# Kernel tuning notes

Measured on AMD Instinct MI355X. Metric: run time of the kernel, lower is better.

Reference implementation:

```python
import jax, jax.numpy as jnp
import numpy as np

H = 15  # hidden_dim


def _lstm_layer(x_seq, w_ih, w_hh, b_ih, b_hh):
    """One LSTM layer, PyTorch gate order (i, f, g, o).
    x_seq: (T, B, D_in) -> returns output sequence (T, B, H)."""
    T, B, _ = x_seq.shape
    # Precompute input contribution for all timesteps at once: (T, B, 4H)
    xw = jnp.einsum('tbd,gd->tbg', x_seq, w_ih) + b_ih + b_hh

    def step(carry, xw_t):
        h, c = carry
        gates = xw_t + h @ w_hh.T  # (B, 4H)
        i, f, g, o = jnp.split(gates, 4, axis=-1)
        i = jax.nn.sigmoid(i)
        f = jax.nn.sigmoid(f)
        g = jnp.tanh(g)
        o = jax.nn.sigmoid(o)
        c = f * c + i * g
        h = o * jnp.tanh(c)
        return (h, c), h

    h0 = jnp.zeros((B, H), dtype=x_seq.dtype)
    c0 = jnp.zeros((B, H), dtype=x_seq.dtype)
    _, out = jax.lax.scan(step, (h0, c0), xw)
    return out  # (T, B, H)


def setup_inputs() -> dict:
    key = jax.random.key(0)
    ks = jax.random.split(key, 11)
    D, OUT = 5, 25
    s = 0.1
    return {
        'x':     jax.random.normal(ks[0], (512, 4096, D), dtype=jnp.float32),
        'w_ih0': jax.random.normal(ks[1], (4 * H, D), dtype=jnp.float32) * s,
        'w_hh0': jax.random.normal(ks[2], (4 * H, H), dtype=jnp.float32) * s,
        'b_ih0': jax.random.normal(ks[3], (4 * H,), dtype=jnp.float32) * s,
        'b_hh0': jax.random.normal(ks[4], (4 * H,), dtype=jnp.float32) * s,
        'w_ih1': jax.random.normal(ks[5], (4 * H, H), dtype=jnp.float32) * s,
        'w_hh1': jax.random.normal(ks[6], (4 * H, H), dtype=jnp.float32) * s,
        'b_ih1': jax.random.normal(ks[7], (4 * H,), dtype=jnp.float32) * s,
        'b_hh1': jax.random.normal(ks[8], (4 * H,), dtype=jnp.float32) * s,
        'w_lin': jax.random.normal(ks[9], (OUT, H), dtype=jnp.float32) * s,
        'b_lin': jax.random.normal(ks[10], (OUT,), dtype=jnp.float32) * s,
    }


def reference(x, w_ih0, w_hh0, b_ih0, b_hh0, w_ih1, w_hh1, b_ih1, b_hh1, w_lin, b_lin):
    out0 = _lstm_layer(x, w_ih0, w_hh0, b_ih0, b_hh0)      # (T, B, H)
    out1 = _lstm_layer(out0, w_ih1, w_hh1, b_ih1, b_hh1)   # (T, B, H)
    # Faithful to the source: output[:, -1, :] with seq-first layout selects
    # the last BATCH element across all timesteps -> (T, H)
    last = out1[:, -1, :]
    return last @ w_lin.T + b_lin  # (T, OUT)
```

## Files before the change

kernel.cpp:

```cpp
#include <hip/hip_runtime.h>

#define T_SEQ 512
#define BATCH 4096
#define D_IN  5
#define H     15
#define G4    60
#define OUTN  25

__device__ __forceinline__ float fast_exp2(float x) {
#if __has_builtin(__builtin_amdgcn_exp2f)
  return __builtin_amdgcn_exp2f(x);
#else
  return exp2f(x);
#endif
}

__device__ __forceinline__ float fast_rcp(float x) {
#if __has_builtin(__builtin_amdgcn_rcpf)
  return __builtin_amdgcn_rcpf(x);
#else
  return 1.0f / x;
#endif
}

__device__ __forceinline__ float rl(float v, int lane) {
  return __int_as_float(__builtin_amdgcn_readlane(__float_as_int(v), lane));
}

template <int K>
__device__ __forceinline__ float qbcast(float v) {
  return __int_as_float(__builtin_amdgcn_update_dpp(
      0, __float_as_int(v), K * 0x55, 0xF, 0xF, true));
}

__global__ void precompute_xw0(const float* __restrict__ x,
                               const float* __restrict__ w_ih0,
                               const float* __restrict__ b_ih0,
                               const float* __restrict__ b_hh0,
                               float* __restrict__ xw0) {
  int idx = blockIdx.x * blockDim.x + threadIdx.x;
  if (idx >= T_SEQ * G4) return;
  int t = idx / G4;
  int g = idx - t * G4;
  const float* xp = x + ((size_t)t * BATCH + (BATCH - 1)) * D_IN;
  float a = b_ih0[g] + b_hh0[g];
#pragma unroll
  for (int d = 0; d < D_IN; ++d) a = fmaf(xp[d], w_ih0[g * D_IN + d], a);
  xw0[idx] = a;
}

__global__ void __launch_bounds__(64, 1)
lstm_serial(const float* __restrict__ xw0,
            const float* __restrict__ w_hh0,
            const float* __restrict__ w_ih1,
            const float* __restrict__ w_hh1,
            const float* __restrict__ b_ih1,
            const float* __restrict__ b_hh1,
            const float* __restrict__ w_lin,
            const float* __restrict__ b_lin,
            float* __restrict__ out) {
  const int lane = threadIdx.x;
  const int ty = lane & 3;
  const int j  = lane >> 2;
  const int g  = (j < H) ? (ty * H + j) : 0;

  float w0[H], wi1[H], wh1[H];
#pragma unroll
  for (int k = 0; k < H; ++k) {
    w0[k]  = w_hh0[g * H + k];
    wi1[k] = w_ih1[g * H + k];
    wh1[k] = w_hh1[g * H + k];
  }
  const float bias1 = b_ih1[g] + b_hh1[g];

  float wl[H];
  {
    int o = (lane < OUTN) ? lane : 0;
#pragma unroll
    for (int k = 0; k < H; ++k) wl[k] = w_lin[o * H + k];
  }
  const float bl = b_lin[(lane < OUTN) ? lane : 0];

  const bool  isT  = (ty == 2);
  const float expc = isT ? -2.8853900817779268f : -1.4426950408889634f;
  const float sc   = isT ? 2.0f : 1.0f;
  const float off  = isT ? -1.0f : 0.0f;
  const float TANH_C = -2.8853900817779268f;

  float c0 = 0.0f, c1 = 0.0f;
  float sh0[H], sh1[H];
#pragma unroll
  for (int k = 0; k < H; ++k) { sh0[k] = 0.0f; sh1[k] = 0.0f; }

  float xw_cur = xw0[g];
  float xw_n1  = xw0[1 * G4 + g];

  for (int t = 0; t < T_SEQ; ++t) {
    int tn = (t + 2 < T_SEQ) ? (t + 2) : 0;
    float xw_n2 = xw0[tn * G4 + g];

    float u3 = 0.0f, u4 = 0.0f, u5 = 0.0f;
#pragma unroll
    for (int k = 0; k < 5; ++k)   u3 = fmaf(wh1[k], sh1[k], u3);
#pragma unroll
    for (int k = 5; k < 10; ++k)  u4 = fmaf(wh1[k], sh1[k], u4);
#pragma unroll
    for (int k = 10; k < 15; ++k) u5 = fmaf(wh1[k], sh1[k], u5);

    float a0 = xw_cur, a1 = 0.0f, a2 = 0.0f;
#pragma unroll
    for (int k = 0; k < 5; ++k)   a0 = fmaf(w0[k], sh0[k], a0);
#pragma unroll
    for (int k = 5; k < 10; ++k)  a1 = fmaf(w0[k], sh0[k], a1);
#pragma unroll
    for (int k = 10; k < 15; ++k) a2 = fmaf(w0[k], sh0[k], a2);
    float a = a0 + (a1 + a2);

    float e = fast_exp2(a * expc);
    float s = fast_rcp(1.0f + e);
    float v = fmaf(s, sc, off);

    float vi = qbcast<0>(v), vf = qbcast<1>(v), vg = qbcast<2>(v), vo = qbcast<3>(v);
    c0 = fmaf(vf, c0, vi * vg);
    float ec = fast_exp2(c0 * TANH_C);
    float th = fmaf(fast_rcp(1.0f + ec), 2.0f, -1.0f);
    float h0v = vo * th;

#pragma unroll
    for (int k = 0; k < H; ++k) sh0[k] = rl(h0v, 4 * k);

    float u0 = bias1, u1 = 0.0f, u2 = 0.0f;
#pragma unroll
    for (int k = 0; k < 5; ++k)   u0 = fmaf(wi1[k], sh0[k], u0);
#pragma unroll
    for (int k = 5; k < 10; ++k)  u1 = fmaf(wi1[k], sh0[k], u1);
#pragma unroll
    for (int k = 10; k < 15; ++k) u2 = fmaf(wi1[k], sh0[k], u2);
    float b = ((u0 + u1) + (u2 + u3)) + (u4 + u5);

    float eb = fast_exp2(b * expc);
    float sb = fast_rcp(1.0f + eb);
    float vb = fmaf(sb, sc, off);

    float qi = qbcast<0>(vb), qf = qbcast<1>(vb), qg = qbcast<2>(vb), qo = qbcast<3>(vb);
    c1 = fmaf(qf, c1, qi * qg);
    float ec1 = fast_exp2(c1 * TANH_C);
    float th1 = fmaf(fast_rcp(1.0f + ec1), 2.0f, -1.0f);
    float h1v = qo * th1;

#pragma unroll
    for (int k = 0; k < H; ++k) sh1[k] = rl(h1v, 4 * k);

    float o0 = bl, o1 = 0.0f, o2 = 0.0f;
#pragma unroll
    for (int k = 0; k < 5; ++k)   o0 = fmaf(wl[k], sh1[k], o0);
#pragma unroll
    for (int k = 5; k < 10; ++k)  o1 = fmaf(wl[k], sh1[k], o1);
#pragma unroll
    for (int k = 10; k < 15; ++k) o2 = fmaf(wl[k], sh1[k], o2);
    if (lane < OUTN) out[t * OUTN + lane] = o0 + (o1 + o2);

    xw_cur = xw_n1;
    xw_n1  = xw_n2;
  }
}

extern "C" void kernel_launch(void* const* d_in, const int* in_sizes, int n_in,
                              void* d_out, int out_size, void* d_ws, size_t ws_size,
                              hipStream_t stream) {
  const float* x     = (const float*)d_in[0];
  const float* w_ih0 = (const float*)d_in[1];
  const float* w_hh0 = (const float*)d_in[2];
  const float* b_ih0 = (const float*)d_in[3];
  const float* b_hh0 = (const float*)d_in[4];
  const float* w_ih1 = (const float*)d_in[5];
  const float* w_hh1 = (const float*)d_in[6];
  const float* b_ih1 = (const float*)d_in[7];
  const float* b_hh1 = (const float*)d_in[8];
  const float* w_lin = (const float*)d_in[9];
  const float* b_lin = (const float*)d_in[10];
  float* out = (float*)d_out;
  float* xw0 = (float*)d_ws;

  precompute_xw0<<<dim3((T_SEQ * G4 + 255) / 256), dim3(256), 0, stream>>>(
      x, w_ih0, b_ih0, b_hh0, xw0);
  lstm_serial<<<dim3(1), dim3(64), 0, stream>>>(
      xw0, w_hh0, w_ih1, w_hh1, b_ih1, b_hh1, w_lin, b_lin, out);
}
```

Measured before the change: 291.2 us.

## Skew LSTM layers across timesteps and fold activation scales into weights

After: 236.9 us. 1.23x faster.

```diff
diff --git a/kernel.cpp b/kernel.cpp
--- a/kernel.cpp
+++ b/kernel.cpp
@@ -6,6 +6,10 @@
 #define H     15
 #define G4    60
 #define OUTN  25
+
+#define LOG2E   1.4426950408889634f
+#define M_SIG  (-1.4426950408889634f)
+#define M_TANH (-2.8853901f)
 
 __device__ __forceinline__ float fast_exp2(float x) {
 #if __has_builtin(__builtin_amdgcn_exp2f)
@@ -46,7 +50,8 @@
   float a = b_ih0[g] + b_hh0[g];
 #pragma unroll
   for (int d = 0; d < D_IN; ++d) a = fmaf(xp[d], w_ih0[g * D_IN + d], a);
-  xw0[idx] = a;
+  float m = (g / H == 2) ? M_TANH : M_SIG;
+  xw0[idx] = a * m;
 }
 
 __global__ void __launch_bounds__(64, 1)
@@ -64,14 +69,19 @@
   const int j  = lane >> 2;
   const int g  = (j < H) ? (ty * H + j) : 0;
 
+  const bool  isT = (ty == 2);
+  const float m   = isT ? M_TANH : M_SIG;
+  const float scv  = isT ? (2.0f * M_TANH) : 1.0f;
+  const float offv = isT ? (-M_TANH) : 0.0f;
+
   float w0[H], wi1[H], wh1[H];
 #pragma unroll
   for (int k = 0; k < H; ++k) {
-    w0[k]  = w_hh0[g * H + k];
-    wi1[k] = w_ih1[g * H + k];
-    wh1[k] = w_hh1[g * H + k];
+    w0[k]  = w_hh0[g * H + k] * m;
+    wi1[k] = w_ih1[g * H + k] * m;
+    wh1[k] = w_hh1[g * H + k] * m;
   }
-  const float bias1 = b_ih1[g] + b_hh1[g];
+  const float bias1 = (b_ih1[g] + b_hh1[g]) * m;
 
   float wl[H];
   {
@@ -81,88 +91,92 @@
   }
   const float bl = b_lin[(lane < OUTN) ? lane : 0];
 
-  const bool  isT  = (ty == 2);
-  const float expc = isT ? -2.8853900817779268f : -1.4426950408889634f;
-  const float sc   = isT ? 2.0f : 1.0f;
-  const float off  = isT ? -1.0f : 0.0f;
-  const float TANH_C = -2.8853900817779268f;
-
   float c0 = 0.0f, c1 = 0.0f;
   float sh0[H], sh1[H];
 #pragma unroll
   for (int k = 0; k < H; ++k) { sh0[k] = 0.0f; sh1[k] = 0.0f; }
 
+  float h0v = 0.0f, h1v = 0.0f;
+
+  auto L0 = [&](float xw) {
+    float a0 = xw, a1 = 0.0f, a2 = 0.0f;
+#pragma unroll
+    for (int k = 0; k < 5; ++k)   a0 = fmaf(w0[k], sh0[k], a0);
+#pragma unroll
+    for (int k = 5; k < 10; ++k)  a1 = fmaf(w0[k], sh0[k], a1);
+#pragma unroll
+    for (int k = 10; k < 15; ++k) a2 = fmaf(w0[k], sh0[k], a2);
+    float a = a0 + (a1 + a2);
+    float e = fast_exp2(a);
+    float s = fast_rcp(1.0f + e);
+    float v = fmaf(s, scv, offv);
+    float vi = qbcast<0>(v), vf = qbcast<1>(v), vg = qbcast<2>(v), vo = qbcast<3>(v);
+    c0 = fmaf(vf, c0, vi * vg);
+    float th = fmaf(fast_rcp(1.0f + fast_exp2(c0)), 2.0f, -1.0f);
+    h0v = vo * th;
+  };
+  auto L1 = [&]() {
+    float u0 = bias1, u1 = 0.0f, u2 = 0.0f, u3 = 0.0f, u4 = 0.0f, u5 = 0.0f;
+#pragma unroll
+    for (int k = 0; k < 5; ++k)   { u0 = fmaf(wi1[k], sh0[k], u0); u3 = fmaf(wh1[k], sh1[k], u3); }
+#pragma unroll
+    for (int k = 5; k < 10; ++k)  { u1 = fmaf(wi1[k], sh0[k], u1); u4 = fmaf(wh1[k], sh1[k], u4); }
+#pragma unroll
+    for (int k = 10; k < 15; ++k) { u2 = fmaf(wi1[k], sh0[k], u2); u5 = fmaf(wh1[k], sh1[k], u5); }
+    float b = ((u0 + u1) + (u2 + u3)) + (u4 + u5);
+    float e = fast_exp2(b);
+    float s = fast_rcp(1.0f + e);
+    float v = fmaf(s, scv, offv);
+    float qi = qbcast<0>(v), qf = qbcast<1>(v), qg = qbcast<2>(v), qo = qbcast<3>(v);
+    c1 = fmaf(qf, c1, qi * qg);
+    float th = fmaf(fast_rcp(1.0f + fast_exp2(c1)), 2.0f, -1.0f);
+    h1v = qo * th;
+  };
+  auto B0 = [&]() {
+#pragma unroll
+    for (int k = 0; k < H; ++k) sh0[k] = rl(h0v, 4 * k);
+  };
+  auto B1 = [&]() {
+#pragma unroll
+    for (int k = 0; k < H; ++k) sh1[k] = rl(h1v, 4 * k);
+  };
+  auto LIN = [&](int t2, bool do_store) {
+    float o0 = bl, o1 = 0.0f, o2 = 0.0f;
+#pragma unroll
+    for (int k = 0; k < 5; ++k)   o0 = fmaf(wl[k], sh1[k], o0);
+#pragma unroll
+    for (int k = 5; k < 10; ++k)  o1 = fmaf(wl[k], sh1[k], o1);
+#pragma unroll
+    for (int k = 10; k < 15; ++k) o2 = fmaf(wl[k], sh1[k], o2);
+    if (do_store && lane < OUTN) out[t2 * OUTN + lane] = o0 + (o1 + o2);
+  };
+
   float xw_cur = xw0[g];
   float xw_n1  = xw0[1 * G4 + g];
-
-  for (int t = 0; t < T_SEQ; ++t) {
-    int tn = (t + 2 < T_SEQ) ? (t + 2) : 0;
+  L0(xw_cur);
+  B0();
+  xw_cur = xw_n1;
+  xw_n1  = xw0[2 * G4 + g];
+
+  for (int i = 1; i < T_SEQ; ++i) {
+    int tn = (i + 2 < T_SEQ) ? (i + 2) : 0;
     float xw_n2 = xw0[tn * G4 + g];
 
-    float u3 = 0.0f, u4 = 0.0f, u5 = 0.0f;
-#pragma unroll
-    for (int k = 0; k < 5; ++k)   u3 = fmaf(wh1[k], sh1[k], u3);
-#pragma unroll
-    for (int k = 5; k < 10; ++k)  u4 = fmaf(wh1[k], sh1[k], u4);
-#pragma unroll
-    for (int k = 10; k < 15; ++k) u5 = fmaf(wh1[k], sh1[k], u5);
-
-    float a0 = xw_cur, a1 = 0.0f, a2 = 0.0f;
-#pragma unroll
-    for (int k = 0; k < 5; ++k)   a0 = fmaf(w0[k], sh0[k], a0);
-#pragma unroll
-    for (int k = 5; k < 10; ++k)  a1 = fmaf(w0[k], sh0[k], a1);
-#pragma unroll
-    for (int k = 10; k < 15; ++k) a2 = fmaf(w0[k], sh0[k], a2);
-    float a = a0 + (a1 + a2);
-
-    float e = fast_exp2(a * expc);
-    float s = fast_rcp(1.0f + e);
-    float v = fmaf(s, sc, off);
-
-    float vi = qbcast<0>(v), vf = qbcast<1>(v), vg = qbcast<2>(v), vo = qbcast<3>(v);
-    c0 = fmaf(vf, c0, vi * vg);
-    float ec = fast_exp2(c0 * TANH_C);
-    float th = fmaf(fast_rcp(1.0f + ec), 2.0f, -1.0f);
-    float h0v = vo * th;
-
-#pragma unroll
-    for (int k = 0; k < H; ++k) sh0[k] = rl(h0v, 4 * k);
-
-    float u0 = bias1, u1 = 0.0f, u2 = 0.0f;
-#pragma unroll
-    for (int k = 0; k < 5; ++k)   u0 = fmaf(wi1[k], sh0[k], u0);
-#pragma unroll
-    for (int k = 5; k < 10; ++k)  u1 = fmaf(wi1[k], sh0[k], u1);
-#pragma unroll
-    for (int k = 10; k < 15; ++k) u2 = fmaf(wi1[k], sh0[k], u2);
-    float b = ((u0 + u1) + (u2 + u3)) + (u4 + u5);
-
-    float eb = fast_exp2(b * expc);
-    float sb = fast_rcp(1.0f + eb);
-    float vb = fmaf(sb, sc, off);
-
-    float qi = qbcast<0>(vb), qf = qbcast<1>(vb), qg = qbcast<2>(vb), qo = qbcast<3>(vb);
-    c1 = fmaf(qf, c1, qi * qg);
-    float ec1 = fast_exp2(c1 * TANH_C);
-    float th1 = fmaf(fast_rcp(1.0f + ec1), 2.0f, -1.0f);
-    float h1v = qo * th1;
-
-#pragma unroll
-    for (int k = 0; k < H; ++k) sh1[k] = rl(h1v, 4 * k);
-
-    float o0 = bl, o1 = 0.0f, o2 = 0.0f;
-#pragma unroll
-    for (int k = 0; k < 5; ++k)   o0 = fmaf(wl[k], sh1[k], o0);
-#pragma unroll
-    for (int k = 5; k < 10; ++k)  o1 = fmaf(wl[k], sh1[k], o1);
-#pragma unroll
-    for (int k = 10; k < 15; ++k) o2 = fmaf(wl[k], sh1[k], o2);
-    if (lane < OUTN) out[t * OUTN + lane] = o0 + (o1 + o2);
+    L1();
+    L0(xw_cur);
+    LIN(i - 2, i >= 2);
+
+    B0();
+    B1();
 
     xw_cur = xw_n1;
     xw_n1  = xw_n2;
   }
+
+  LIN(T_SEQ - 2, true);
+  L1();
+  B1();
+  LIN(T_SEQ - 1, true);
 }
 
 extern "C" void kernel_launch(void* const* d_in, const int* in_sizes, int n_in,
```
